# Optimization experiments

Hardware: AMD Instinct MI355X
Metric: run time of the kernel (lower is better)

## Reference

```python
import jax, jax.numpy as jnp
import numpy as np

HEADS = 16
KEY_SIZE = 64
SIZE_PER_HEAD = 64
OUT_DIM = HEADS * SIZE_PER_HEAD  # 1024
BIG = 1e10
B, LQ, LK = 2, 2048, 2048


def setup_inputs() -> dict:
    key = jax.random.key(0)
    ks = jax.random.split(key, 8)
    q = jax.random.normal(ks[0], (B, LQ, OUT_DIM), dtype=jnp.float32)
    k = jax.random.normal(ks[1], (B, LK, OUT_DIM), dtype=jnp.float32)
    v = jax.random.normal(ks[2], (B, LK, OUT_DIM), dtype=jnp.float32)
    v_mask = (jax.random.uniform(ks[3], (B, LK)) > 0.1).astype(jnp.float32)
    q_mask = (jax.random.uniform(ks[4], (B, LQ)) > 0.1).astype(jnp.float32)
    # bias-free Linear weights, torch layout [out_features, in_features]
    s = 1.0 / np.sqrt(OUT_DIM)
    Wq = jax.random.normal(ks[5], (HEADS * KEY_SIZE, OUT_DIM), dtype=jnp.float32) * s
    Wk = jax.random.normal(ks[6], (HEADS * KEY_SIZE, OUT_DIM), dtype=jnp.float32) * s
    Wv = jax.random.normal(ks[7], (OUT_DIM, OUT_DIM), dtype=jnp.float32) * s
    return {"q": q, "k": k, "v": v, "v_mask": v_mask, "q_mask": q_mask,
            "Wq": Wq, "Wk": Wk, "Wv": Wv}


def _attention(q, k, v, v_mask, q_mask, Wq, Wk, Wv):
    b, lq, _ = q.shape
    lk = k.shape[1]
    # projections (torch Linear: x @ W.T)
    qw = jnp.einsum('bld,ed->ble', q, Wq).reshape(b, lq, HEADS, KEY_SIZE)
    kw = jnp.einsum('bld,ed->ble', k, Wk).reshape(b, lk, HEADS, KEY_SIZE)
    vw = jnp.einsum('bld,ed->ble', v, Wv).reshape(b, lk, HEADS, SIZE_PER_HEAD)
    # scores [B, H, Lq, Lk]
    a = jnp.einsum('bqhd,bkhd->bhqk', qw, kw) / np.sqrt(KEY_SIZE).astype(np.float32)
    # additive key-padding mask: a - (1 - v_mask) * BIG, broadcast over H and Lq
    a = a - (1.0 - v_mask)[:, None, None, :] * BIG
    # mask_right=True branch: mask = (1 - triu(ones, diag=1)) * BIG, i.e. lower
    # triangle INCLUDING the diagonal is penalized (faithful to source quirk).
    causal = jnp.tril(jnp.ones((lq, lk), dtype=a.dtype)) * BIG  # [Lq, Lk]
    a = a - causal[None, None, :, :]
    a = jax.nn.softmax(a, axis=-1)
    # output [B, Lq, H*dv]
    o = jnp.einsum('bhqk,bkhd->bqhd', a, vw).reshape(b, lq, OUT_DIM)
    o = o * q_mask[:, :, None]
    return o


def reference(q, k, v, v_mask, q_mask, Wq, Wk, Wv):
    return _attention(q, k, v, v_mask, q_mask, Wq, Wk, Wv)
```

## Files before the change

kernel.cpp:

```cpp
#include <hip/hip_runtime.h>
#include <hip/hip_bf16.h>
#include <stdint.h>

#define B_    2
#define SEQ   2048
#define EMB   1024
#define BIGF  1e10f
#define LOG2E 1.4426950408889634f
#define BIG2F (1e10f * LOG2E)
#define C2    (0.125f * LOG2E)

typedef unsigned short u16;
typedef __attribute__((ext_vector_type(4))) u16      u16x4;
typedef __attribute__((ext_vector_type(8))) short    bf8;
typedef __attribute__((ext_vector_type(4))) float    f4;
typedef __attribute__((ext_vector_type(4))) float    fv4;

__device__ inline float bf2f(u16 u){ union{uint32_t i; float f;} v; v.i = ((uint32_t)u) << 16; return v.f; }
__device__ inline u16 f2bf(float f){ union{float f; uint32_t i;} v; v.f = f;
                                     uint32_t r = v.i + 0x7fffu + ((v.i >> 16) & 1u); return (u16)(r >> 16); }
__device__ inline float exp2_hw(float x){ float r; asm("v_exp_f32 %0, %1" : "=v"(r) : "v"(x)); return r; }

__device__ inline void gl_lds16(const void* g, void* l){
  __builtin_amdgcn_global_load_lds((const __attribute__((address_space(1))) uint32_t*)g,
                                   (__attribute__((address_space(3))) uint32_t*)l, 16, 0, 0);
}

struct CvtArgs { const float* src[6]; u16* dst[6]; int n[6]; };

__global__ __launch_bounds__(256) void cvt_bf16(CvtArgs a)
{
  const int seg = blockIdx.y;
  const float* __restrict__ s = a.src[seg];
  u16* __restrict__ d = a.dst[seg];
  const int n = a.n[seg];
  const int i = (blockIdx.x * 256 + threadIdx.x) * 8;
  if (i >= n) return;
  fv4 x0 = *(const fv4*)(s + i);
  fv4 x1 = *(const fv4*)(s + i + 4);
  union { bf8 v; u16 u[8]; } o;
#pragma unroll
  for (int j = 0; j < 4; j++) { o.u[j] = f2bf(x0[j]); o.u[4 + j] = f2bf(x1[j]); }
  *(bf8*)(d + i) = o.v;
}

__global__ __launch_bounds__(256) void proj_gemm(
    const u16* __restrict__ Xq, const u16* __restrict__ Xk, const u16* __restrict__ Xv,
    const u16* __restrict__ Wq, const u16* __restrict__ Wk, const u16* __restrict__ Wv,
    u16* __restrict__ QH, u16* __restrict__ KH, u16* __restrict__ VTB)
{
  __shared__ u16 smem[18432];
  u16* lA = smem;
  u16* lB = smem + 4096;

  const int z = blockIdx.z;
  const u16* X = (z == 0) ? Xq : ((z == 1) ? Xk : Xv);
  const u16* W = (z == 0) ? Wq : ((z == 1) ? Wk : Wv);

  const int tid  = threadIdx.x;
  const int lane = tid & 63;
  const int w    = tid >> 6;
  const int wm   = w >> 1, wn = w & 1;
  const int m0   = blockIdx.x * 128;
  const int n0   = blockIdx.y * 128;

  const f4 zero = {0.f, 0.f, 0.f, 0.f};
  f4 acc[4][4];
#pragma unroll
  for (int i = 0; i < 4; i++)
#pragma unroll
    for (int j = 0; j < 4; j++) acc[i][j] = zero;

  for (int k0 = 0; k0 < 1024; k0 += 32) {
    __syncthreads();
#pragma unroll
    for (int j = 0; j < 2; j++) {
      const int c = j * 256 + tid;
      const int row = c >> 2, cc = (c & 3) * 8;
      gl_lds16(X + (size_t)(m0 + row) * 1024 + k0 + cc, &lA[(j * 256 + w * 64) * 8]);
      gl_lds16(W + (size_t)(n0 + row) * 1024 + k0 + cc, &lB[(j * 256 + w * 64) * 8]);
    }
    __syncthreads();
    const int koff = (lane >> 4) * 8;
    bf8 a[4], b[4];
#pragma unroll
    for (int t = 0; t < 4; t++) a[t] = *(const bf8*)&lA[(wm * 64 + t * 16 + (lane & 15)) * 32 + koff];
#pragma unroll
    for (int t = 0; t < 4; t++) b[t] = *(const bf8*)&lB[(wn * 64 + t * 16 + (lane & 15)) * 32 + koff];
#pragma unroll
    for (int mt = 0; mt < 4; mt++)
#pragma unroll
      for (int nt = 0; nt < 4; nt++)
        acc[mt][nt] = __builtin_amdgcn_mfma_f32_16x16x32_bf16(a[mt], b[nt], acc[mt][nt], 0, 0, 0);
  }

  __syncthreads();
  const int col = lane & 15, quad = lane >> 4;
  u16* ep = &smem[w * 4608];

  if (z == 2) {
#pragma unroll
    for (int mt = 0; mt < 4; mt++)
#pragma unroll
      for (int nt = 0; nt < 4; nt++) {
        u16x4 pk = { f2bf(acc[mt][nt][0]), f2bf(acc[mt][nt][1]),
                     f2bf(acc[mt][nt][2]), f2bf(acc[mt][nt][3]) };
        *(u16x4*)&ep[(nt * 16 + col) * 72 + mt * 16 + quad * 4] = pk;
      }
  } else {
#pragma unroll
    for (int mt = 0; mt < 4; mt++)
#pragma unroll
      for (int nt = 0; nt < 4; nt++)
#pragma unroll
        for (int r = 0; r < 4; r++)
          ep[(mt * 16 + quad * 4 + r) * 72 + nt * 16 + col] = f2bf(acc[mt][nt][r]);
  }

  const int bb = m0 >> 11;
  const int h  = (n0 >> 6) + wn;
  const int bh = bb * 16 + h;

  if (z == 0) {
    const int qbase = (m0 & 2047) + wm * 64;
    u16* dst = QH + ((size_t)bh * SEQ + qbase) * 64;
#pragma unroll
    for (int i = 0; i < 8; i++) {
      const int f  = i * 1024 + lane * 16;
      const int ml = i * 8 + (lane >> 3), nl = (lane & 7) * 8;
      *(bf8*)(dst + (f >> 1)) = *(const bf8*)&ep[ml * 72 + nl];
    }
  } else if (z == 1) {
    const int kt = (((m0 & 2047) >> 6) + wm);
    u16* dst = KH + (((size_t)bh * 32 + kt) << 12);
#pragma unroll
    for (int i = 0; i < 8; i++) {
      const int f   = i * 1024 + lane * 16;
      const int dh  = f >> 12;
      const int klc = (f >> 6) & 63;
      const int dlo = (lane & 3) * 8;
      *(bf8*)(dst + (f >> 1)) = *(const bf8*)&ep[klc * 72 + dh * 32 + dlo];
    }
  } else {
    const int kt = (((m0 & 2047) >> 6) + wm);
    u16* dst = VTB + (((size_t)bh * 32 + kt) << 12);
#pragma unroll
    for (int i = 0; i < 8; i++) {
      const int f   = i * 1024 + lane * 16;
      const int kk  = f >> 12;
      const int d   = (f >> 6) & 63;
      const int klo = (lane & 3) * 8;
      *(bf8*)(dst + (f >> 1)) = *(const bf8*)&ep[d * 72 + kk * 32 + klo];
    }
  }
}

__global__ __launch_bounds__(256) void sumv(const u16* __restrict__ VTB,
                                            const float* __restrict__ vmask,
                                            float* __restrict__ fb)
{
  const int w = threadIdx.x >> 6, lane = threadIdx.x & 63;
  const int gw = blockIdx.x * 4 + w;
  const int b = gw >> 10, e = gw & 1023;
  const int h = e >> 6, d = e & 63;
  const int bh = b * 16 + h;
  const float* vm = vmask + b * SEQ;
  float s = 0.f, c = 0.f;
  for (int kt = 0; kt < 32; kt++) {
    const u16 val = VTB[(((size_t)bh * 32 + kt) << 12) + (lane >> 5) * 2048 + d * 32 + (lane & 31)];
    const float m = vm[kt * 64 + lane];
    s += m * bf2f(val); c += m;
  }
#pragma unroll
  for (int o = 1; o < 64; o <<= 1) { s += __shfl_xor(s, o); c += __shfl_xor(c, o); }
  if (lane == 0) fb[gw] = s / c;
}

__global__ __launch_bounds__(256) void attn(
    const u16* __restrict__ QH, const u16* __restrict__ KH, const u16* __restrict__ VTB,
    const float* __restrict__ vmask, const float* __restrict__ qmask,
    const float* __restrict__ fb, float* __restrict__ OUT)
{
  __shared__ float pen[SEQ];
  __shared__ u16   sK[2][4096];
  __shared__ u16   sV[2][4096];
  __shared__ u16   P[4 * 16 * 72];

  const int tid = threadIdx.x, lane = tid & 63, w = tid >> 6;
  const int i   = blockIdx.x;
  const int xcd = i & 7;
  const int j   = i >> 3;
  const int bh  = xcd + 8 * (j >> 4);
  const int qpair = j & 15;
  const int b = bh >> 4, h = bh & 15;
  const int col = lane & 15, quad = lane >> 4;
  const int wb = w * 16 * 72;

  for (int t = tid; t < SEQ; t += 256)
    pen[t] = (1.0f - vmask[b * SEQ + t]) * BIG2F;

  const u16* kbase = KH  + (((size_t)bh * 32) << 12);
  const u16* vbase = VTB + (((size_t)bh * 32) << 12);

  for (int pass = 0; pass < 2; pass++) {
    const int qx = pass ? (31 - qpair) : qpair;
    const int q0 = qx * 64;

    bf8 aQ[2];
#pragma unroll
    for (int dh = 0; dh < 2; dh++)
      aQ[dh] = *(const bf8*)&QH[((size_t)bh * SEQ + q0 + w * 16 + col) * 64 + dh * 32 + quad * 8];

    const f4 zero = {0.f, 0.f, 0.f, 0.f};
    f4 accO[4];
    float l_part[4] = {0.f, 0.f, 0.f, 0.f};
#pragma unroll
    for (int t = 0; t < 4; t++) accO[t] = zero;

    __syncthreads();
    {
      const size_t toff = ((size_t)qx << 12) + w * 1024 + lane * 8;
      gl_lds16(kbase + toff,       &sK[0][w * 1024]);
      gl_lds16(kbase + toff + 512, &sK[0][w * 1024 + 512]);
      gl_lds16(vbase + toff,       &sV[0][w * 1024]);
      gl_lds16(vbase + toff + 512, &sV[0][w * 1024 + 512]);
    }

    const int ntile = 32 - qx;
    for (int it = 0; it < ntile; it++) {
      __syncthreads();
      if (it + 1 < ntile) {
        const int nb = (it + 1) & 1;
        const size_t toff = ((size_t)(qx + it + 1) << 12) + w * 1024 + lane * 8;
        gl_lds16(kbase + toff,       &sK[nb][w * 1024]);
        gl_lds16(kbase + toff + 512, &sK[nb][w * 1024 + 512]);
        gl_lds16(vbase + toff,       &sV[nb][w * 1024]);
        gl_lds16(vbase + toff + 512, &sV[nb][w * 1024 + 512]);
      }
      const u16* cK = sK[it & 1];
      const u16* cV = sV[it & 1];
      const int k0 = (qx + it) * 64;

      f4 accS[4];
#pragma unroll
      for (int t = 0; t < 4; t++) accS[t] = zero;
#pragma unroll
      for (int nt = 0; nt < 4; nt++)
#pragma unroll
        for (int dh = 0; dh < 2; dh++) {
          bf8 bK = *(const bf8*)&cK[dh * 2048 + (nt * 16 + col) * 32 + quad * 8];
          accS[nt] = __builtin_amdgcn_mfma_f32_16x16x32_bf16(aQ[dh], bK, accS[nt], 0, 0, 0);
        }

      float pen4[4];
#pragma unroll
      for (int nt = 0; nt < 4; nt++) pen4[nt] = pen[k0 + nt * 16 + col];
      float p[4][4];
      if (it == 0) {
#pragma unroll
        for (int nt = 0; nt < 4; nt++)
#pragma unroll
          for (int r = 0; r < 4; r++) {
            float sv = fmaf(accS[nt][r], C2, -pen4[nt]);
            if (nt * 16 + col <= w * 16 + quad * 4 + r) sv -= BIG2F;
            p[nt][r] = exp2_hw(sv);
          }
      } else {
#pragma unroll
        for (int nt = 0; nt < 4; nt++)
#pragma unroll
          for (int r = 0; r < 4; r++)
            p[nt][r] = exp2_hw(fmaf(accS[nt][r], C2, -pen4[nt]));
      }
#pragma unroll
      for (int r = 0; r < 4; r++)
        l_part[r] += (p[0][r] + p[1][r]) + (p[2][r] + p[3][r]);

#pragma unroll
      for (int nt = 0; nt < 4; nt++)
#pragma unroll
        for (int rp = 0; rp < 4; rp += 2) {
          float2 f2c; f2c.x = p[nt][rp]; f2c.y = p[nt][rp + 1];
          union { __hip_bfloat162 h2; u16 u[2]; } cv;
          cv.h2 = __float22bfloat162_rn(f2c);
          P[wb + (quad * 4 + rp    ) * 72 + nt * 16 + col] = cv.u[0];
          P[wb + (quad * 4 + rp + 1) * 72 + nt * 16 + col] = cv.u[1];
        }

#pragma unroll
      for (int kk = 0; kk < 2; kk++) {
        bf8 aP = *(const bf8*)&P[wb + col * 72 + kk * 32 + quad * 8];
#pragma unroll
        for (int nt = 0; nt < 4; nt++) {
          bf8 bV = *(const bf8*)&cV[kk * 2048 + (nt * 16 + col) * 32 + quad * 8];
          accO[nt] = __builtin_amdgcn_mfma_f32_16x16x32_bf16(aP, bV, accO[nt], 0, 0, 0);
        }
      }
    }

#pragma unroll
    for (int r = 0; r < 4; r++) {
      float l = l_part[r];
      l += __shfl_xor(l, 1); l += __shfl_xor(l, 2);
      l += __shfl_xor(l, 4); l += __shfl_xor(l, 8);
      const int q = q0 + w * 16 + quad * 4 + r;
      const float qm = qmask[b * SEQ + q];
      float* op = OUT + (size_t)(b * SEQ + q) * EMB + h * 64;
      if (l == 0.0f) {
#pragma unroll
        for (int nt = 0; nt < 4; nt++)
          op[nt * 16 + col] = fb[b * 1024 + h * 64 + nt * 16 + col] * qm;
      } else {
        const float s = qm / l;
#pragma unroll
        for (int nt = 0; nt < 4; nt++)
          op[nt * 16 + col] = accO[nt][r] * s;
      }
    }
  }
}

extern "C" void kernel_launch(void* const* d_in, const int* in_sizes, int n_in,
                              void* d_out, int out_size, void* d_ws, size_t ws_size,
                              hipStream_t stream)
{
  const float* q  = (const float*)d_in[0];
  const float* k  = (const float*)d_in[1];
  const float* v  = (const float*)d_in[2];
  const float* vm = (const float*)d_in[3];
  const float* qm = (const float*)d_in[4];
  const float* Wq = (const float*)d_in[5];
  const float* Wk = (const float*)d_in[6];
  const float* Wv = (const float*)d_in[7];
  float* out = (float*)d_out;

  const size_t NBIG = (size_t)B_ * SEQ * EMB;
  const size_t NW   = (size_t)EMB * EMB;

  u16* qb  = (u16*)d_ws;
  u16* kb  = qb  + NBIG;
  u16* vb  = kb  + NBIG;
  u16* Wqb = vb  + NBIG;
  u16* Wkb = Wqb + NW;
  u16* Wvb = Wkb + NW;
  u16* QH  = Wvb + NW;
  u16* KH  = QH  + NBIG;
  u16* VTB = KH  + NBIG;
  float* fb = (float*)(VTB + NBIG);

  CvtArgs ca;
  ca.src[0] = q;  ca.dst[0] = qb;  ca.n[0] = (int)NBIG;
  ca.src[1] = k;  ca.dst[1] = kb;  ca.n[1] = (int)NBIG;
  ca.src[2] = v;  ca.dst[2] = vb;  ca.n[2] = (int)NBIG;
  ca.src[3] = Wq; ca.dst[3] = Wqb; ca.n[3] = (int)NW;
  ca.src[4] = Wk; ca.dst[4] = Wkb; ca.n[4] = (int)NW;
  ca.src[5] = Wv; ca.dst[5] = Wvb; ca.n[5] = (int)NW;

  cvt_bf16<<<dim3((unsigned)(NBIG / 8 / 256), 6, 1), 256, 0, stream>>>(ca);
  proj_gemm<<<dim3(32, 8, 3), 256, 0, stream>>>(qb, kb, vb, Wqb, Wkb, Wvb, QH, KH, VTB);
  sumv<<<dim3(512, 1, 1), 256, 0, stream>>>(VTB, vm, fb);
  attn<<<dim3(512, 1, 1), 256, 0, stream>>>(QH, KH, VTB, vm, qm, fb, out);
}
```

Baseline: 204.4 us.

## Transpose attention MFMA operands and double projection GEMM K-step

The attention kernel swaps MFMA operand roles to compute S^T and O^T. Each lane then owns one query row with four contiguous keys or output columns. This enables vectorized penalty loads, packed 4-wide bf16 stores of P, a two-step shuffle row-sum instead of four four-step sums, and float4 output stores. Separately, the projection GEMM now loads a 64-wide K slab per barrier pair, halving the number of synchronizations at the cost of more LDS per block.

```diff
diff --git a/kernel.cpp b/kernel.cpp
--- a/kernel.cpp
+++ b/kernel.cpp
@@ -51,7 +51,7 @@
 {
   __shared__ u16 smem[18432];
   u16* lA = smem;
-  u16* lB = smem + 4096;
+  u16* lB = smem + 8192;
 
   const int z = blockIdx.z;
   const u16* X = (z == 0) ? Xq : ((z == 1) ? Xk : Xv);
@@ -63,6 +63,7 @@
   const int wm   = w >> 1, wn = w & 1;
   const int m0   = blockIdx.x * 128;
   const int n0   = blockIdx.y * 128;
+  const int col  = lane & 15, quad = lane >> 4;
 
   const f4 zero = {0.f, 0.f, 0.f, 0.f};
   f4 acc[4][4];
@@ -71,31 +72,35 @@
 #pragma unroll
     for (int j = 0; j < 4; j++) acc[i][j] = zero;
 
-  for (int k0 = 0; k0 < 1024; k0 += 32) {
+  for (int k0 = 0; k0 < 1024; k0 += 64) {
     __syncthreads();
 #pragma unroll
-    for (int j = 0; j < 2; j++) {
-      const int c = j * 256 + tid;
-      const int row = c >> 2, cc = (c & 3) * 8;
-      gl_lds16(X + (size_t)(m0 + row) * 1024 + k0 + cc, &lA[(j * 256 + w * 64) * 8]);
-      gl_lds16(W + (size_t)(n0 + row) * 1024 + k0 + cc, &lB[(j * 256 + w * 64) * 8]);
+    for (int j = 0; j < 4; j++) {
+      const int kk  = j >> 1;
+      const int row = (j & 1) * 64 + w * 16 + (lane >> 2);
+      const int cc  = (lane & 3) * 8;
+      const size_t g = (size_t)row * 1024 + k0 + kk * 32 + cc;
+      gl_lds16(X + (size_t)m0 * 1024 + g, &lA[(j * 256 + w * 64) * 8]);
+      gl_lds16(W + (size_t)n0 * 1024 + g, &lB[(j * 256 + w * 64) * 8]);
     }
     __syncthreads();
-    const int koff = (lane >> 4) * 8;
-    bf8 a[4], b[4];
-#pragma unroll
-    for (int t = 0; t < 4; t++) a[t] = *(const bf8*)&lA[(wm * 64 + t * 16 + (lane & 15)) * 32 + koff];
-#pragma unroll
-    for (int t = 0; t < 4; t++) b[t] = *(const bf8*)&lB[(wn * 64 + t * 16 + (lane & 15)) * 32 + koff];
-#pragma unroll
-    for (int mt = 0; mt < 4; mt++)
-#pragma unroll
-      for (int nt = 0; nt < 4; nt++)
-        acc[mt][nt] = __builtin_amdgcn_mfma_f32_16x16x32_bf16(a[mt], b[nt], acc[mt][nt], 0, 0, 0);
+#pragma unroll
+    for (int kk = 0; kk < 2; kk++) {
+      const int koff = kk * 4096 + quad * 8;
+      bf8 a[4], b[4];
+#pragma unroll
+      for (int t = 0; t < 4; t++) a[t] = *(const bf8*)&lA[koff + (wm * 64 + t * 16 + col) * 32];
+#pragma unroll
+      for (int t = 0; t < 4; t++) b[t] = *(const bf8*)&lB[koff + (wn * 64 + t * 16 + col) * 32];
+#pragma unroll
+      for (int mt = 0; mt < 4; mt++)
+#pragma unroll
+        for (int nt = 0; nt < 4; nt++)
+          acc[mt][nt] = __builtin_amdgcn_mfma_f32_16x16x32_bf16(a[mt], b[nt], acc[mt][nt], 0, 0, 0);
+    }
   }
 
   __syncthreads();
-  const int col = lane & 15, quad = lane >> 4;
   u16* ep = &smem[w * 4608];
 
   if (z == 2) {
@@ -206,14 +211,14 @@
     const int qx = pass ? (31 - qpair) : qpair;
     const int q0 = qx * 64;
 
-    bf8 aQ[2];
+    bf8 bQ[2];
 #pragma unroll
     for (int dh = 0; dh < 2; dh++)
-      aQ[dh] = *(const bf8*)&QH[((size_t)bh * SEQ + q0 + w * 16 + col) * 64 + dh * 32 + quad * 8];
+      bQ[dh] = *(const bf8*)&QH[((size_t)bh * SEQ + q0 + w * 16 + col) * 64 + dh * 32 + quad * 8];
 
     const f4 zero = {0.f, 0.f, 0.f, 0.f};
     f4 accO[4];
-    float l_part[4] = {0.f, 0.f, 0.f, 0.f};
+    float l_acc = 0.f;
 #pragma unroll
     for (int t = 0; t < 4; t++) accO[t] = zero;
 
@@ -248,21 +253,21 @@
       for (int nt = 0; nt < 4; nt++)
 #pragma unroll
         for (int dh = 0; dh < 2; dh++) {
-          bf8 bK = *(const bf8*)&cK[dh * 2048 + (nt * 16 + col) * 32 + quad * 8];
-          accS[nt] = __builtin_amdgcn_mfma_f32_16x16x32_bf16(aQ[dh], bK, accS[nt], 0, 0, 0);
+          bf8 aK = *(const bf8*)&cK[dh * 2048 + (nt * 16 + col) * 32 + quad * 8];
+          accS[nt] = __builtin_amdgcn_mfma_f32_16x16x32_bf16(aK, bQ[dh], accS[nt], 0, 0, 0);
         }
 
-      float pen4[4];
-#pragma unroll
-      for (int nt = 0; nt < 4; nt++) pen4[nt] = pen[k0 + nt * 16 + col];
       float p[4][4];
+      fv4 pv[4];
+#pragma unroll
+      for (int nt = 0; nt < 4; nt++) pv[nt] = *(const fv4*)&pen[k0 + nt * 16 + quad * 4];
       if (it == 0) {
 #pragma unroll
         for (int nt = 0; nt < 4; nt++)
 #pragma unroll
           for (int r = 0; r < 4; r++) {
-            float sv = fmaf(accS[nt][r], C2, -pen4[nt]);
-            if (nt * 16 + col <= w * 16 + quad * 4 + r) sv -= BIG2F;
+            float sv = fmaf(accS[nt][r], C2, -pv[nt][r]);
+            if (nt * 16 + quad * 4 + r <= w * 16 + col) sv -= BIG2F;
             p[nt][r] = exp2_hw(sv);
           }
       } else {
@@ -270,51 +275,53 @@
         for (int nt = 0; nt < 4; nt++)
 #pragma unroll
           for (int r = 0; r < 4; r++)
-            p[nt][r] = exp2_hw(fmaf(accS[nt][r], C2, -pen4[nt]));
-      }
-#pragma unroll
-      for (int r = 0; r < 4; r++)
-        l_part[r] += (p[0][r] + p[1][r]) + (p[2][r] + p[3][r]);
-
+            p[nt][r] = exp2_hw(fmaf(accS[nt][r], C2, -pv[nt][r]));
+      }
 #pragma unroll
       for (int nt = 0; nt < 4; nt++)
-#pragma unroll
-        for (int rp = 0; rp < 4; rp += 2) {
-          float2 f2c; f2c.x = p[nt][rp]; f2c.y = p[nt][rp + 1];
-          union { __hip_bfloat162 h2; u16 u[2]; } cv;
-          cv.h2 = __float22bfloat162_rn(f2c);
-          P[wb + (quad * 4 + rp    ) * 72 + nt * 16 + col] = cv.u[0];
-          P[wb + (quad * 4 + rp + 1) * 72 + nt * 16 + col] = cv.u[1];
+        l_acc += (p[nt][0] + p[nt][1]) + (p[nt][2] + p[nt][3]);
+
+#pragma unroll
+      for (int nt = 0; nt < 4; nt++) {
+        union { u16x4 v; u16 u[4]; } pk;
+        union { __hip_bfloat162 h2; u16 u[2]; } c0, c1;
+        float2 f01; f01.x = p[nt][0]; f01.y = p[nt][1];
+        float2 f23; f23.x = p[nt][2]; f23.y = p[nt][3];
+        c0.h2 = __float22bfloat162_rn(f01);
+        c1.h2 = __float22bfloat162_rn(f23);
+        pk.u[0] = c0.u[0]; pk.u[1] = c0.u[1]; pk.u[2] = c1.u[0]; pk.u[3] = c1.u[1];
+        *(u16x4*)&P[wb + col * 72 + nt * 16 + quad * 4] = pk.v;
+      }
+
+#pragma unroll
+      for (int kk = 0; kk < 2; kk++) {
+        bf8 bP = *(const bf8*)&P[wb + col * 72 + kk * 32 + quad * 8];
+#pragma unroll
+        for (int nt = 0; nt < 4; nt++) {
+          bf8 aV = *(const bf8*)&cV[kk * 2048 + (nt * 16 + col) * 32 + quad * 8];
+          accO[nt] = __builtin_amdgcn_mfma_f32_16x16x32_bf16(aV, bP, accO[nt], 0, 0, 0);
         }
-
-#pragma unroll
-      for (int kk = 0; kk < 2; kk++) {
-        bf8 aP = *(const bf8*)&P[wb + col * 72 + kk * 32 + quad * 8];
-#pragma unroll
-        for (int nt = 0; nt < 4; nt++) {
-          bf8 bV = *(const bf8*)&cV[kk * 2048 + (nt * 16 + col) * 32 + quad * 8];
-          accO[nt] = __builtin_amdgcn_mfma_f32_16x16x32_bf16(aP, bV, accO[nt], 0, 0, 0);
-        }
-      }
-    }
-
-#pragma unroll
-    for (int r = 0; r < 4; r++) {
-      float l = l_part[r];
-      l += __shfl_xor(l, 1); l += __shfl_xor(l, 2);
-      l += __shfl_xor(l, 4); l += __shfl_xor(l, 8);
-      const int q = q0 + w * 16 + quad * 4 + r;
-      const float qm = qmask[b * SEQ + q];
-      float* op = OUT + (size_t)(b * SEQ + q) * EMB + h * 64;
-      if (l == 0.0f) {
-#pragma unroll
-        for (int nt = 0; nt < 4; nt++)
-          op[nt * 16 + col] = fb[b * 1024 + h * 64 + nt * 16 + col] * qm;
-      } else {
-        const float s = qm / l;
-#pragma unroll
-        for (int nt = 0; nt < 4; nt++)
-          op[nt * 16 + col] = accO[nt][r] * s;
+      }
+    }
+
+    float l = l_acc;
+    l += __shfl_xor(l, 16); l += __shfl_xor(l, 32);
+    const int q = q0 + w * 16 + col;
+    const float qm = qmask[b * SEQ + q];
+    float* op = OUT + (size_t)(b * SEQ + q) * EMB + h * 64;
+    if (l == 0.0f) {
+#pragma unroll
+      for (int nt = 0; nt < 4; nt++) {
+        fv4 f = *(const fv4*)&fb[b * 1024 + h * 64 + nt * 16 + quad * 4];
+        f *= qm;
+        *(fv4*)(op + nt * 16 + quad * 4) = f;
+      }
+    } else {
+      const float s = qm / l;
+#pragma unroll
+      for (int nt = 0; nt < 4; nt++) {
+        fv4 f = { accO[nt][0] * s, accO[nt][1] * s, accO[nt][2] * s, accO[nt][3] * s };
+        *(fv4*)(op + nt * 16 + quad * 4) = f;
       }
     }
   }
```

Result: faster. 199.9 us (-2.2%).
